# Kernel tuning notes

Measured on AMD Instinct MI355X. Metric: run time of the kernel, lower is better.

Reference implementation:

```python
import jax, jax.numpy as jnp
import numpy as np

N = 131072   # nodes
C = 128      # in_channels
R = 4        # num_residues
H = 128      # hidden_channels
B = 1024     # graphs (segments)
QS = jnp.arange(1, 10, dtype=jnp.float32) * 0.1  # quantiles 0.1..0.9


def setup_inputs() -> dict:
    key = jax.random.key(0)
    ks = jax.random.split(key, 12)
    s = 0.05
    return {
        "embedding_0": jax.random.normal(ks[0], (N, C, 1, R), jnp.float32),
        "batch": jnp.sort(jax.random.randint(ks[1], (N,), 0, B, dtype=jnp.int32)),
        "W_lins": jax.random.normal(ks[2], (R - 1, C), jnp.float32) * s,
        "b_lins": jax.random.normal(ks[3], (R - 1,), jnp.float32) * s,
        "W1": jax.random.normal(ks[4], (C, H), jnp.float32) * s,
        "b1": jax.random.normal(ks[5], (H,), jnp.float32) * s,
        "W2": jax.random.normal(ks[6], (H,), jnp.float32) * s,
        "b2": jax.random.normal(ks[7], (1,), jnp.float32) * s,
        "Wm1": jax.random.normal(ks[8], (12, H), jnp.float32) * s,
        "bm1": jax.random.normal(ks[9], (H,), jnp.float32) * s,
        "Wm2": jax.random.normal(ks[10], (H,), jnp.float32) * s,
        "bm2": jax.random.normal(ks[11], (1,), jnp.float32) * s,
    }


def _node_readout(emb, W_lins, b_lins, W1, b1, W2, b2):
    x = emb[:, :, 0, :]                         # [N, C, R]
    # sum of (num_residues-1) plain linears, each Linear(C, 1)
    lin = jnp.einsum('ncr,rc->n', x[:, :, :-1], W_lins) + jnp.sum(b_lins)
    # non-linear branch on last residue: Linear(C,H) -> relu -> Linear(H,1)
    h = jax.nn.relu(x[:, :, -1] @ W1 + b1)      # [N, H]
    nl = h @ W2 + b2                            # [N]
    return lin + nl                             # [N]


def _multi_aggregate(v, batch):
    ones = jnp.ones_like(v)
    counts_f = jax.ops.segment_sum(ones, batch, num_segments=B)        # [B]
    counts = counts_f.astype(jnp.int32)
    safe_cnt = jnp.maximum(counts_f, 1.0)
    mean = jax.ops.segment_sum(v, batch, num_segments=B) / safe_cnt
    mx = jax.ops.segment_max(v, batch, num_segments=B)
    mn = jax.ops.segment_min(v, batch, num_segments=B)
    # per-segment sort (batch is primary key, value secondary)
    order = jnp.lexsort((v, batch))
    vs = v[order]                                                      # segment-sorted values
    offsets = jnp.concatenate([jnp.zeros(1, jnp.int32), jnp.cumsum(counts)[:-1].astype(jnp.int32)])
    last = offsets + jnp.maximum(counts, 1) - 1                        # last valid index per segment
    # linear-interpolated quantiles: pos = q*(count-1) within each segment
    pos = QS[:, None] * (safe_cnt[None, :] - 1.0)                      # [9, B]
    f = jnp.floor(pos).astype(jnp.int32)
    frac = pos - f.astype(jnp.float32)
    lo_idx = jnp.clip(offsets[None, :] + f, offsets[None, :], last[None, :])
    hi_idx = jnp.clip(lo_idx + 1, offsets[None, :], last[None, :])
    quant = vs[lo_idx] + frac * (vs[hi_idx] - vs[lo_idx])              # [9, B]
    nonempty = (counts > 0)[:, None]
    agg = jnp.concatenate([mean[:, None], mx[:, None], mn[:, None], quant.T], axis=1)  # [B, 12]
    return jnp.where(nonempty, agg, 0.0)


def reference(embedding_0, batch, W_lins, b_lins, W1, b1, W2, b2, Wm1, bm1, Wm2, bm2):
    batch = batch.astype(jnp.int32)
    v = _node_readout(embedding_0, W_lins, b_lins, W1, b1, W2, b2)     # [N]
    agg = _multi_aggregate(v, batch)                                   # [B, 12]
    out = jax.nn.relu(agg @ Wm1 + bm1) @ Wm2 + bm2                     # [B]
    return out
```

## Files before the change

kernel.cpp:

```cpp
#include <hip/hip_runtime.h>
#include <stdint.h>

#define N_NODES 131072
#define C_DIM   128
#define H_DIM   128
#define B_SEG   1024
#define M_TILE  128
#define K_TILE  32
#define YT_STR  132
#define SEGCAP  384

#define GLOAD_LDS16(gaddr, laddr)                                              \
    __builtin_amdgcn_global_load_lds(                                          \
        (const __attribute__((address_space(1))) void*)(gaddr),                \
        (__attribute__((address_space(3))) void*)(laddr), 16, 0, 0)

__global__ __launch_bounds__(256, 4)
void node_readout_kernel(const float* __restrict__ emb,
                         const float* __restrict__ W_lins,
                         const float* __restrict__ b_lins,
                         const float* __restrict__ W1,
                         const float* __restrict__ b1,
                         const float* __restrict__ W2,
                         const float* __restrict__ b2,
                         float* __restrict__ v_out)
{
    __shared__ float Yt[K_TILE * YT_STR];
    __shared__ float W1s[K_TILE * H_DIM];
    __shared__ float WLs[3 * C_DIM];
    __shared__ float lin_lds[M_TILE];

    const int t  = threadIdx.x;
    const int nbase = blockIdx.x * M_TILE;
    const int ln = t >> 5;
    const int cc = t & 31;
    const int jg = t & 15;
    const int mg = t >> 4;
    const int w  = t >> 6;

    for (int i = t; i < 3 * C_DIM; i += 256) WLs[i] = W_lins[i];

    float acc[8][8];
    #pragma unroll
    for (int mi = 0; mi < 8; ++mi)
        #pragma unroll
        for (int ji = 0; ji < 8; ++ji) acc[mi][ji] = 0.0f;

    float lin_p[16];
    #pragma unroll
    for (int p = 0; p < 16; ++p) lin_p[p] = 0.0f;

    const float4* xbase = (const float4*)emb + (size_t)(nbase + ln) * C_DIM;

    const int ct0 = (blockIdx.x ^ (blockIdx.x >> 8)) & 3;

    __syncthreads();

    for (int it = 0; it < C_DIM / K_TILE; ++it) {
        const int ct = (it + ct0) & 3;
        if (it) __syncthreads();

        const int c0 = ct * K_TILE + cc;
        const float wl0 = WLs[c0], wl1 = WLs[C_DIM + c0], wl2 = WLs[2 * C_DIM + c0];

        float4 xp[4];
        #pragma unroll
        for (int i = 0; i < 4; ++i)
            xp[i] = xbase[i * 8 * C_DIM + ct * K_TILE + cc];

        {
            const char* wsrc = (const char*)(W1 + ct * (K_TILE * H_DIM));
            char*       wdst = (char*)W1s;
            #pragma unroll
            for (int q = 0; q < 4; ++q) {
                GLOAD_LDS16(wsrc + (size_t)(q * 256 + t) * 16,
                            wdst + (size_t)(q * 256 + w * 64) * 16);
            }
        }

        #pragma unroll
        for (int p = 0; p < 16; ++p) {
            float4 x = xp[p & 3];
            if (p < 12)
                xp[p & 3] = xbase[(p + 4) * 8 * C_DIM + ct * K_TILE + cc];
            lin_p[p] = fmaf(x.x, wl0, fmaf(x.y, wl1, fmaf(x.z, wl2, lin_p[p])));
            Yt[cc * YT_STR + p * 8 + ln] = x.w;
        }

        __syncthreads();

        #pragma unroll 8
        for (int k = 0; k < K_TILE; ++k) {
            float4 ya = *(const float4*)&Yt[k * YT_STR + mg * 8];
            float4 yb = *(const float4*)&Yt[k * YT_STR + mg * 8 + 4];
            float wv[8];
            #pragma unroll
            for (int ji = 0; ji < 8; ++ji) wv[ji] = W1s[k * H_DIM + jg + 16 * ji];
            float ym[8] = {ya.x, ya.y, ya.z, ya.w, yb.x, yb.y, yb.z, yb.w};
            #pragma unroll
            for (int mi = 0; mi < 8; ++mi)
                #pragma unroll
                for (int ji = 0; ji < 8; ++ji)
                    acc[mi][ji] = fmaf(ym[mi], wv[ji], acc[mi][ji]);
        }
    }

    #pragma unroll
    for (int p = 0; p < 16; ++p) {
        float s = lin_p[p];
        s += __shfl_xor(s, 16);
        s += __shfl_xor(s, 8);
        s += __shfl_xor(s, 4);
        s += __shfl_xor(s, 2);
        s += __shfl_xor(s, 1);
        lin_p[p] = s;
    }
    if (cc == 0) {
        #pragma unroll
        for (int p = 0; p < 16; ++p) lin_lds[p * 8 + ln] = lin_p[p];
    }

    __syncthreads();
    float* nl_red = W1s;

    float b1r[8], W2r[8];
    #pragma unroll
    for (int ji = 0; ji < 8; ++ji) {
        int j = jg + 16 * ji;
        b1r[ji] = b1[j];
        W2r[ji] = W2[j];
    }

    #pragma unroll
    for (int mi = 0; mi < 8; ++mi) {
        float s = 0.0f;
        #pragma unroll
        for (int ji = 0; ji < 8; ++ji) {
            float h = acc[mi][ji] + b1r[ji];
            h = h > 0.0f ? h : 0.0f;
            s = fmaf(h, W2r[ji], s);
        }
        nl_red[(mg * 8 + mi) * 17 + jg] = s;
    }
    __syncthreads();

    if (t < M_TILE) {
        float s = lin_lds[t];
        #pragma unroll
        for (int g = 0; g < 16; ++g) s += nl_red[t * 17 + g];
        s += b_lins[0] + b_lins[1] + b_lins[2] + b2[0];
        v_out[nbase + t] = s;
    }
}

__device__ __forceinline__ int lower_bound_wave(const int* __restrict__ batch,
                                                int target, int lane)
{
    int lo = 0, hi = N_NODES;
    while (lo < hi) {
        int span  = hi - lo;
        int chunk = (span + 63) >> 6;
        int idx   = lo + lane * chunk;
        bool p    = (idx < hi) && (batch[idx] < target);
        unsigned long long m = __ballot(p);
        int c = __popcll(m);
        if (c == 0) return lo;
        int nhi = (c < 64) ? (lo + c * chunk) : hi;
        lo = lo + (c - 1) * chunk + 1;
        hi = (nhi < hi) ? nhi : hi;
    }
    return lo;
}

__global__ __launch_bounds__(256)
void aggregate_kernel(const float* __restrict__ v,
                      const int* __restrict__ batch,
                      const float* __restrict__ Wm1,
                      const float* __restrict__ bm1,
                      const float* __restrict__ Wm2,
                      const float* __restrict__ bm2,
                      float* __restrict__ out)
{
    __shared__ float vals[4][SEGCAP];
    __shared__ float sorted[4][SEGCAP];
    __shared__ float agg_s[4][12];

    const int t    = threadIdx.x;
    const int wid  = t >> 6;
    const int lane = t & 63;
    const int b    = blockIdx.x * 4 + wid;

    const int start = lower_bound_wave(batch, b, lane);
    const int end   = lower_bound_wave(batch, b + 1, lane);
    int cnt = end - start;
    if (cnt > SEGCAP) cnt = SEGCAP;

    float lsum = 0.0f;
    for (int i = lane; i < cnt; i += 64) {
        float x = v[start + i];
        vals[wid][i] = x;
        lsum += x;
    }
    #pragma unroll
    for (int o = 32; o; o >>= 1) lsum += __shfl_xor(lsum, o);
    __syncthreads();

    for (int i = lane; i < cnt; i += 64) {
        float xi = vals[wid][i];
        int r = 0;
        for (int j = 0; j < cnt; ++j) {
            float xj = vals[wid][j];
            r += (xj < xi) || (xj == xi && j < i);
        }
        sorted[wid][r] = xi;
    }
    __syncthreads();

    if (cnt > 0) {
        float cntf = (float)cnt;
        if (lane == 9)  agg_s[wid][0] = lsum / cntf;
        if (lane == 10) agg_s[wid][1] = sorted[wid][cnt - 1];
        if (lane == 11) agg_s[wid][2] = sorted[wid][0];
        if (lane < 9) {
            float q   = (float)(lane + 1) * 0.1f;
            float pos = q * (cntf - 1.0f);
            float f   = floorf(pos);
            float frac = pos - f;
            int loi = (int)f;
            int hii = loi + 1; if (hii > cnt - 1) hii = cnt - 1;
            agg_s[wid][3 + lane] = sorted[wid][loi] + frac * (sorted[wid][hii] - sorted[wid][loi]);
        }
    } else {
        if (lane < 12) agg_s[wid][lane] = 0.0f;
    }
    __syncthreads();

    float term = 0.0f;
    #pragma unroll
    for (int rj = 0; rj < 2; ++rj) {
        int j = lane + 64 * rj;
        float h = bm1[j];
        #pragma unroll
        for (int k = 0; k < 12; ++k) h = fmaf(agg_s[wid][k], Wm1[k * H_DIM + j], h);
        h = h > 0.0f ? h : 0.0f;
        term = fmaf(h, Wm2[j], term);
    }
    #pragma unroll
    for (int o = 32; o; o >>= 1) term += __shfl_xor(term, o);
    if (lane == 0) out[b] = term + bm2[0];
}

extern "C" void kernel_launch(void* const* d_in, const int* in_sizes, int n_in,
                              void* d_out, int out_size, void* d_ws, size_t ws_size,
                              hipStream_t stream)
{
    const float* emb    = (const float*)d_in[0];
    const int*   batch  = (const int*)d_in[1];
    const float* W_lins = (const float*)d_in[2];
    const float* b_lins = (const float*)d_in[3];
    const float* W1     = (const float*)d_in[4];
    const float* b1     = (const float*)d_in[5];
    const float* W2     = (const float*)d_in[6];
    const float* b2     = (const float*)d_in[7];
    const float* Wm1    = (const float*)d_in[8];
    const float* bm1    = (const float*)d_in[9];
    const float* Wm2    = (const float*)d_in[10];
    const float* bm2    = (const float*)d_in[11];

    float* out  = (float*)d_out;
    float* vbuf = (float*)d_ws;

    node_readout_kernel<<<N_NODES / M_TILE, 256, 0, stream>>>(
        emb, W_lins, b_lins, W1, b1, W2, b2, vbuf);
    aggregate_kernel<<<B_SEG / 4, 256, 0, stream>>>(
        vbuf, batch, Wm1, bm1, Wm2, bm2, out);
}
```

Baseline: 417.2 us.

## Double-buffer LDS tiles to overlap next-tile loads with FMA compute

Double-buffers the LDS tiles for the transposed last-residue activations and the W1 slice. The next K-tile's global loads, linear-branch FMAs and LDS stores are interleaved with the current tile's outer-product FMA loop. This removes one barrier per iteration and hides global latency behind compute. In exchange LDS use doubles and launch bounds drop to 2 blocks per CU, so occupancy is lower and register pressure higher.

```diff
diff --git a/kernel.cpp b/kernel.cpp
--- a/kernel.cpp
+++ b/kernel.cpp
@@ -15,7 +15,7 @@
         (const __attribute__((address_space(1))) void*)(gaddr),                \
         (__attribute__((address_space(3))) void*)(laddr), 16, 0, 0)
 
-__global__ __launch_bounds__(256, 4)
+__global__ __launch_bounds__(256, 2)
 void node_readout_kernel(const float* __restrict__ emb,
                          const float* __restrict__ W_lins,
                          const float* __restrict__ b_lins,
@@ -25,8 +25,8 @@
                          const float* __restrict__ b2,
                          float* __restrict__ v_out)
 {
-    __shared__ float Yt[K_TILE * YT_STR];
-    __shared__ float W1s[K_TILE * H_DIM];
+    __shared__ float Yt[2][K_TILE * YT_STR];
+    __shared__ float W1s[2][K_TILE * H_DIM];
     __shared__ float WLs[3 * C_DIM];
     __shared__ float lin_lds[M_TILE];
 
@@ -54,55 +54,79 @@
 
     const int ct0 = (blockIdx.x ^ (blockIdx.x >> 8)) & 3;
 
-    __syncthreads();
-
-    for (int it = 0; it < C_DIM / K_TILE; ++it) {
-        const int ct = (it + ct0) & 3;
-        if (it) __syncthreads();
-
-        const int c0 = ct * K_TILE + cc;
-        const float wl0 = WLs[c0], wl1 = WLs[C_DIM + c0], wl2 = WLs[2 * C_DIM + c0];
-
-        float4 xp[4];
-        #pragma unroll
-        for (int i = 0; i < 4; ++i)
-            xp[i] = xbase[i * 8 * C_DIM + ct * K_TILE + cc];
-
-        {
-            const char* wsrc = (const char*)(W1 + ct * (K_TILE * H_DIM));
-            char*       wdst = (char*)W1s;
+    {
+        const char* wsrc = (const char*)(W1 + ct0 * (K_TILE * H_DIM));
+        char*       wdst = (char*)&W1s[0][0];
+        #pragma unroll
+        for (int q = 0; q < 4; ++q)
+            GLOAD_LDS16(wsrc + (size_t)(q * 256 + t) * 16,
+                        wdst + (size_t)(q * 256 + w * 64) * 16);
+    }
+    const int c00 = ct0 * K_TILE + cc;
+    float4 xp[4];
+    #pragma unroll
+    for (int i = 0; i < 4; ++i) xp[i] = xbase[i * 8 * C_DIM + c00];
+
+    __syncthreads();
+
+    {
+        const float wl0 = WLs[c00], wl1 = WLs[C_DIM + c00], wl2 = WLs[2 * C_DIM + c00];
+        #pragma unroll
+        for (int p = 0; p < 16; ++p) {
+            float4 x = xp[p & 3];
+            if (p < 12) xp[p & 3] = xbase[(p + 4) * 8 * C_DIM + c00];
+            lin_p[p] = fmaf(x.x, wl0, fmaf(x.y, wl1, fmaf(x.z, wl2, lin_p[p])));
+            Yt[0][cc * YT_STR + p * 8 + ln] = x.w;
+        }
+    }
+    __syncthreads();
+
+    for (int it = 0; it < 4; ++it) {
+        const int cur = it & 1;
+        const int ctn = (it + 1 + ct0) & 3;
+        const bool pf = (it < 3);
+        const int c0n = ctn * K_TILE + cc;
+
+        if (pf) {
+            const char* wsrc = (const char*)(W1 + ctn * (K_TILE * H_DIM));
+            char*       wdst = (char*)&W1s[cur ^ 1][0];
             #pragma unroll
-            for (int q = 0; q < 4; ++q) {
+            for (int q = 0; q < 4; ++q)
                 GLOAD_LDS16(wsrc + (size_t)(q * 256 + t) * 16,
                             wdst + (size_t)(q * 256 + w * 64) * 16);
+            #pragma unroll
+            for (int i = 0; i < 4; ++i) xp[i] = xbase[i * 8 * C_DIM + c0n];
+        }
+        const float wl0 = WLs[c0n], wl1 = WLs[C_DIM + c0n], wl2 = WLs[2 * C_DIM + c0n];
+
+        #pragma unroll
+        for (int q = 0; q < 4; ++q) {
+            #pragma unroll
+            for (int k = q * 8; k < q * 8 + 8; ++k) {
+                float4 ya = *(const float4*)&Yt[cur][k * YT_STR + mg * 8];
+                float4 yb = *(const float4*)&Yt[cur][k * YT_STR + mg * 8 + 4];
+                float wv[8];
+                #pragma unroll
+                for (int ji = 0; ji < 8; ++ji) wv[ji] = W1s[cur][k * H_DIM + jg + 16 * ji];
+                float ym[8] = {ya.x, ya.y, ya.z, ya.w, yb.x, yb.y, yb.z, yb.w};
+                #pragma unroll
+                for (int mi = 0; mi < 8; ++mi)
+                    #pragma unroll
+                    for (int ji = 0; ji < 8; ++ji)
+                        acc[mi][ji] = fmaf(ym[mi], wv[ji], acc[mi][ji]);
             }
-        }
-
-        #pragma unroll
-        for (int p = 0; p < 16; ++p) {
-            float4 x = xp[p & 3];
-            if (p < 12)
-                xp[p & 3] = xbase[(p + 4) * 8 * C_DIM + ct * K_TILE + cc];
-            lin_p[p] = fmaf(x.x, wl0, fmaf(x.y, wl1, fmaf(x.z, wl2, lin_p[p])));
-            Yt[cc * YT_STR + p * 8 + ln] = x.w;
-        }
-
+            if (pf) {
+                #pragma unroll
+                for (int i = 0; i < 4; ++i) {
+                    const int p = q * 4 + i;
+                    float4 x = xp[i];
+                    if (p < 12) xp[i] = xbase[(p + 4) * 8 * C_DIM + c0n];
+                    lin_p[p] = fmaf(x.x, wl0, fmaf(x.y, wl1, fmaf(x.z, wl2, lin_p[p])));
+                    Yt[cur ^ 1][cc * YT_STR + p * 8 + ln] = x.w;
+                }
+            }
+        }
         __syncthreads();
-
-        #pragma unroll 8
-        for (int k = 0; k < K_TILE; ++k) {
-            float4 ya = *(const float4*)&Yt[k * YT_STR + mg * 8];
-            float4 yb = *(const float4*)&Yt[k * YT_STR + mg * 8 + 4];
-            float wv[8];
-            #pragma unroll
-            for (int ji = 0; ji < 8; ++ji) wv[ji] = W1s[k * H_DIM + jg + 16 * ji];
-            float ym[8] = {ya.x, ya.y, ya.z, ya.w, yb.x, yb.y, yb.z, yb.w};
-            #pragma unroll
-            for (int mi = 0; mi < 8; ++mi)
-                #pragma unroll
-                for (int ji = 0; ji < 8; ++ji)
-                    acc[mi][ji] = fmaf(ym[mi], wv[ji], acc[mi][ji]);
-        }
     }
 
     #pragma unroll
@@ -121,7 +145,7 @@
     }
 
     __syncthreads();
-    float* nl_red = W1s;
+    float* nl_red = &W1s[0][0];
 
     float b1r[8], W2r[8];
     #pragma unroll
```

Result: slower. 1.172 ms (+180.8%).
